# Performance work log

Measured on AMD Instinct MI355X. Metric: run time of the kernel, lower is better.

The kernel has to match this reference:

```python
import jax, jax.numpy as jnp
import numpy as np

EDGE_WIDTH = 128
NUM_HEADS = 8
LN_EPS = 1e-5


def setup_inputs() -> dict:
    key = jax.random.key(0)
    ks = jax.random.split(key, 8)
    B, N, C, H = 2, 512, EDGE_WIDTH, NUM_HEADS
    e = jax.random.normal(ks[0], (B, N, N, C), dtype=jnp.float32)
    mask = jnp.zeros((B, N, N, 1), dtype=jnp.float32)
    s = 0.05
    return {
        "e": e,
        "mask": mask,
        "ln_w": jnp.ones((C,), dtype=jnp.float32),
        "ln_b": jnp.zeros((C,), dtype=jnp.float32),
        "Wv": jax.random.normal(ks[1], (C, 4 * H), dtype=jnp.float32) * s,
        "bv": jnp.zeros((4 * H,), dtype=jnp.float32),
        "We": jax.random.normal(ks[2], (C, 4 * H), dtype=jnp.float32) * s,
        "be": jnp.zeros((4 * H,), dtype=jnp.float32),
        "Wo": jax.random.normal(ks[3], (2 * H, 2 * C), dtype=jnp.float32) * s,
        "bo": jnp.zeros((2 * C,), dtype=jnp.float32),
    }


def siglin(g, l):
    return jax.nn.sigmoid(g) * l


def reference(e, mask, ln_w, ln_b, Wv, bv, We, be, Wo, bo):
    H = NUM_HEADS
    # LayerNorm over edge_width
    mu = jnp.mean(e, axis=-1, keepdims=True)
    var = jnp.var(e, axis=-1, keepdims=True)
    e_ln = (e - mu) * jax.lax.rsqrt(var + LN_EPS) * ln_w + ln_b
    V = e_ln @ Wv + bv
    E = e_ln @ We + be
    V_in_g, V_in_l, V_out_g, V_out_l = jnp.split(V, 4, axis=-1)
    E_in_g, E_in_l, E_out_g, E_out_l = jnp.split(E, 4, axis=-1)
    V_in = siglin(V_in_g + mask, V_in_l)
    V_out = siglin(V_out_g + mask, V_out_l)
    E_in = siglin(E_in_g + mask, E_in_l)
    E_out = siglin(E_out_g + mask, E_out_l)
    # triangular updates: contract over k per head
    Va_in = jnp.einsum('bikh,bjkh->bijh', E_in, V_in)
    Va_out = jnp.einsum('bkih,bkjh->bijh', E_out, V_out)
    Va = jnp.concatenate([Va_in, Va_out], axis=-1)  # [B,N,N,2H]
    O = Va @ Wo + bo  # [B,N,N,2C]
    e_g, e_l = jnp.split(O, 2, axis=-1)
    return siglin(e_g, e_l)
```

## Files before the change

kernel.cpp:

```cpp
#include <hip/hip_runtime.h>
#include <stdint.h>

#define N_    512
#define C_    128
#define NN_   (N_ * N_)
#define ROWS_ (2 * NN_)
#define GATE_ ((long)2 * 8 * NN_)

typedef __attribute__((ext_vector_type(8))) short short8;
typedef __attribute__((ext_vector_type(4))) float f32x4;
typedef __attribute__((ext_vector_type(4))) unsigned uint4_t;
typedef __attribute__((ext_vector_type(2))) unsigned uint2_t;
typedef unsigned short u16;

static __device__ __forceinline__ u16 f2bf(float f) {
    union { float f; unsigned u; } v; v.f = f;
    unsigned r = v.u + 0x7fffu + ((v.u >> 16) & 1u);
    return (u16)(r >> 16);
}
static __device__ __forceinline__ float bf2f(u16 h) {
    union { unsigned u; float f; } v; v.u = ((unsigned)h) << 16;
    return v.f;
}
static __device__ __forceinline__ float sigmoidf_(float x) {
    return __builtin_amdgcn_rcpf(1.0f + __expf(-x));
}

__global__ __launch_bounds__(256) void k_prep(
    const float* __restrict__ Wv, const float* __restrict__ We,
    const float* __restrict__ Wo, u16* __restrict__ WB, u16* __restrict__ WoB)
{
    int gid = blockIdx.x * 256 + threadIdx.x;
    if (gid < 1024) {
        int chunk = gid >> 6, li = gid & 63;
        int kc = chunk >> 2, ct = chunk & 3;
        int qq = li >> 4, nn = li & 15, c = ct * 16 + nn;
        short8 v;
#pragma unroll
        for (int j = 0; j < 8; ++j) {
            int k = kc * 32 + qq * 8 + j;
            float w = (c < 32) ? Wv[k * 32 + c] : We[k * 32 + (c - 32)];
            v[j] = (short)f2bf(w);
        }
        *(short8*)(&WB[gid * 8]) = v;
    } else if (gid < 3072) {
        int g = gid - 1024;
        int ctp = g >> 6, li = g & 63;
        int ct = ctp & 15, part = ctp >> 4;
        int qq = li >> 4, nn = li & 15, col = ct * 16 + nn;
        short8 v;
#pragma unroll
        for (int j = 0; j < 8; ++j) {
            int k = qq * 8 + j;
            if (k < 16) {
                float w = Wo[k * 256 + col];
                u16 hi = f2bf(w);
                v[j] = part ? (short)f2bf(w - bf2f(hi)) : (short)hi;
            } else v[j] = 0;
        }
        *(short8*)(&WoB[g * 8]) = v;
    }
}

__global__ __launch_bounds__(256) void k_lnproj(
    const float* __restrict__ e, const float* __restrict__ mask,
    const float* __restrict__ lnw, const float* __restrict__ lnb,
    const float* __restrict__ bv, const float* __restrict__ be,
    const u16* __restrict__ WB,
    u16* __restrict__ Vin, u16* __restrict__ Vout,
    u16* __restrict__ Ein, u16* __restrict__ Eout)
{
    const int t = threadIdx.x;
    const int w = t >> 6, l = t & 63;
    const int l15 = l & 15, q = l >> 4;
    const long R0 = (long)blockIdx.x * 64;

    const long Rg = R0 + w * 16 + l15;
    const float* erow = e + Rg * C_ + q * 8;
    float x[32];
#pragma unroll
    for (int kc = 0; kc < 4; ++kc) {
        float4 a = *(const float4*)(erow + kc * 32);
        float4 b = *(const float4*)(erow + kc * 32 + 4);
        x[kc*8+0] = a.x; x[kc*8+1] = a.y; x[kc*8+2] = a.z; x[kc*8+3] = a.w;
        x[kc*8+4] = b.x; x[kc*8+5] = b.y; x[kc*8+6] = b.z; x[kc*8+7] = b.w;
    }
    float s = 0.f, s2 = 0.f;
#pragma unroll
    for (int i = 0; i < 32; ++i) { s += x[i]; s2 += x[i] * x[i]; }
    s  += __shfl_xor(s, 16);  s2 += __shfl_xor(s2, 16);
    s  += __shfl_xor(s, 32);  s2 += __shfl_xor(s2, 32);
    float mu   = s * (1.f / 128.f);
    float var  = s2 * (1.f / 128.f) - mu * mu;
    float rstd = rsqrtf(var + 1e-5f);

    short8 af[4];
#pragma unroll
    for (int kc = 0; kc < 4; ++kc) {
        const float* lwp = lnw + kc * 32 + q * 8;
        const float* lbp = lnb + kc * 32 + q * 8;
        float4 w0 = *(const float4*)lwp, w1 = *(const float4*)(lwp + 4);
        float4 b0 = *(const float4*)lbp, b1 = *(const float4*)(lbp + 4);
        float ww[8] = {w0.x,w0.y,w0.z,w0.w,w1.x,w1.y,w1.z,w1.w};
        float bb[8] = {b0.x,b0.y,b0.z,b0.w,b1.x,b1.y,b1.z,b1.w};
#pragma unroll
        for (int j = 0; j < 8; ++j)
            af[kc][j] = (short)f2bf((x[kc*8+j] - mu) * rstd * ww[j] + bb[j]);
    }

    f32x4 acc[4];
#pragma unroll
    for (int ct = 0; ct < 4; ++ct) acc[ct] = (f32x4){0.f, 0.f, 0.f, 0.f};
#pragma unroll
    for (int kc = 0; kc < 4; ++kc) {
#pragma unroll
        for (int ct = 0; ct < 4; ++ct) {
            short8 bf = *(const short8*)(WB + ((kc * 4 + ct) * 64 + l) * 8);
            acc[ct] = __builtin_amdgcn_mfma_f32_16x16x32_bf16(af[kc], bf, acc[ct], 0, 0, 0);
        }
    }

    float mrow[4];
#pragma unroll
    for (int r = 0; r < 4; ++r) mrow[r] = mask[R0 + w * 16 + q * 4 + r];
    const bool is_gate = (l15 & 8) == 0;
    const int h = l15 & 7;
    const long bb_ = R0 >> 18;
    const long rem0 = (R0 & (NN_ - 1)) + w * 16 + q * 4;
    u16* bufs[4] = { Vin, Vout, Ein, Eout };
#pragma unroll
    for (int ct = 0; ct < 4; ++ct) {
        int cc = (ct * 16 + l15) & 31;
        float bias = (ct < 2) ? bv[cc] : be[cc];
        float vals[4];
#pragma unroll
        for (int r = 0; r < 4; ++r) {
            float val = acc[ct][r] + bias;
            float partner = __shfl_xor(val, 8);
            vals[r] = partner * sigmoidf_(val + mrow[r]);
        }
        if (is_gate) {
            uint2_t p;
            p[0] = (unsigned)f2bf(vals[0]) | ((unsigned)f2bf(vals[1]) << 16);
            p[1] = (unsigned)f2bf(vals[2]) | ((unsigned)f2bf(vals[3]) << 16);
            *(uint2_t*)(bufs[ct] + (bb_ * 8 + h) * (long)NN_ + rem0) = p;
        }
    }
}

__global__ __launch_bounds__(256) void k_tri(
    const u16* __restrict__ Vin, const u16* __restrict__ Vout,
    const u16* __restrict__ Ein, const u16* __restrict__ Eout,
    u16* __restrict__ Va)
{
    __shared__ __align__(16) u16 lA[128 * 72];
    __shared__ __align__(16) u16 lB[128 * 72];
    const int bid = blockIdx.x;
    const int tj = bid & 3, ti = (bid >> 2) & 3, fl = (bid >> 4) & 1;
    const int h = (bid >> 5) & 7, b = (bid >> 8) & 1;
    const u16* Ap = (fl ? Eout : Ein) + (long)(b * 8 + h) * NN_;
    const u16* Bp = (fl ? Vout : Vin) + (long)(b * 8 + h) * NN_;
    u16* Cp = Va + (long)(b * 16 + fl * 8 + h) * NN_;

    const int t = threadIdx.x;
    const int w = t >> 6, l = t & 63, l15 = l & 15, q = l >> 4;
    const int rt = (w >> 1) * 64, ctl = (w & 1) * 64;

    f32x4 acc[4][4];
#pragma unroll
    for (int rr = 0; rr < 4; ++rr)
#pragma unroll
        for (int cc = 0; cc < 4; ++cc) acc[rr][cc] = (f32x4){0.f, 0.f, 0.f, 0.f};

    for (int ks = 0; ks < 512; ks += 64) {
        if (fl == 0) {
#pragma unroll
            for (int p = 0; p < 4; ++p) {
                int cid = t + p * 256;
                int r = cid >> 3, seg = cid & 7;
                *(uint4_t*)(&lA[r * 72 + seg * 8]) =
                    *(const uint4_t*)(Ap + (long)(ti * 128 + r) * 512 + ks + seg * 8);
                *(uint4_t*)(&lB[r * 72 + seg * 8]) =
                    *(const uint4_t*)(Bp + (long)(tj * 128 + r) * 512 + ks + seg * 8);
            }
        } else {
            const u16* P = (t < 128) ? Ap : Bp;
            u16* L = (t < 128) ? lA : lB;
            const int tt = t & 127, ib = tt & 15, kb = tt >> 4;
            const int io = ((t < 128) ? ti : tj) * 128 + ib * 8;
            uint4_t o[8];
#pragma unroll
            for (int p2 = 0; p2 < 4; ++p2) {
                uint4_t ra = *(const uint4_t*)(P + (long)(ks + kb * 8 + 2 * p2    ) * 512 + io);
                uint4_t rb = *(const uint4_t*)(P + (long)(ks + kb * 8 + 2 * p2 + 1) * 512 + io);
#pragma unroll
                for (int d = 0; d < 4; ++d) {
                    o[2*d  ][p2] = __builtin_amdgcn_perm(rb[d], ra[d], 0x05040100u);
                    o[2*d+1][p2] = __builtin_amdgcn_perm(rb[d], ra[d], 0x07060302u);
                }
            }
#pragma unroll
            for (int j = 0; j < 8; ++j)
                *(uint4_t*)(&L[(ib * 8 + j) * 72 + kb * 8]) = o[j];
        }
        __syncthreads();
#pragma unroll
        for (int kf = 0; kf < 2; ++kf) {
            short8 a[4], bf[4];
#pragma unroll
            for (int rr = 0; rr < 4; ++rr)
                a[rr] = *(const short8*)(&lA[(rt + rr * 16 + l15) * 72 + kf * 32 + q * 8]);
#pragma unroll
            for (int cc = 0; cc < 4; ++cc)
                bf[cc] = *(const short8*)(&lB[(ctl + cc * 16 + l15) * 72 + kf * 32 + q * 8]);
#pragma unroll
            for (int rr = 0; rr < 4; ++rr)
#pragma unroll
                for (int cc = 0; cc < 4; ++cc)
                    acc[rr][cc] = __builtin_amdgcn_mfma_f32_16x16x32_bf16(a[rr], bf[cc], acc[rr][cc], 0, 0, 0);
        }
        __syncthreads();
    }
#pragma unroll
    for (int rr = 0; rr < 4; ++rr)
#pragma unroll
        for (int cc = 0; cc < 4; ++cc)
#pragma unroll
            for (int r = 0; r < 4; ++r) {
                int row = ti * 128 + rt + rr * 16 + q * 4 + r;
                int col = tj * 128 + ctl + cc * 16 + l15;
                Cp[(long)row * 512 + col] = f2bf(acc[rr][cc][r]);
            }
}

__global__ __launch_bounds__(256) void k_out(
    const u16* __restrict__ Va, const u16* __restrict__ WoB,
    const float* __restrict__ bo, float* __restrict__ out)
{
    __shared__ __align__(16) u16 lWoB[2048 * 8];
    __shared__ __align__(16) u16 lVa[64 * 32];
    const int t = threadIdx.x;
    const int w = t >> 6, l = t & 63, l15 = l & 15, q = l >> 4;
    const long R0 = (long)blockIdx.x * 64;
    const long bb = R0 >> 18;
    const long rem0 = R0 & (NN_ - 1);

#pragma unroll
    for (int i2 = 0; i2 < 8; ++i2)
        ((uint4_t*)lWoB)[i2 * 256 + t] = ((const uint4_t*)WoB)[i2 * 256 + t];
    {
        int p = t >> 2, j4 = (t & 3) * 4;
        uint2_t z; z[0] = 0; z[1] = 0;
        *(uint2_t*)(&lVa[p * 32 + 16 + j4]) = z;
    }
    {
        int ch = t >> 4, p0 = (t & 15) * 4;
        uint2_t v = *(const uint2_t*)(Va + (bb * 16 + ch) * (long)NN_ + rem0 + p0);
        u16* pv = (u16*)&v;
#pragma unroll
        for (int i = 0; i < 4; ++i) lVa[(p0 + i) * 32 + ch] = pv[i];
    }
    __syncthreads();

    short8 af = *(const short8*)(&lVa[(w * 16 + l15) * 32 + q * 8]);
    f32x4 acc[16];
#pragma unroll
    for (int ct = 0; ct < 16; ++ct) acc[ct] = (f32x4){0.f, 0.f, 0.f, 0.f};
#pragma unroll
    for (int ct = 0; ct < 16; ++ct) {
        short8 bh = *(const short8*)(&lWoB[(ct * 64 + l) * 8]);
        short8 blo = *(const short8*)(&lWoB[((16 + ct) * 64 + l) * 8]);
        acc[ct] = __builtin_amdgcn_mfma_f32_16x16x32_bf16(af, bh, acc[ct], 0, 0, 0);
        acc[ct] = __builtin_amdgcn_mfma_f32_16x16x32_bf16(af, blo, acc[ct], 0, 0, 0);
    }

#pragma unroll
    for (int ct = 0; ct < 8; ++ct) {
        int cg = ct * 16 + l15;
        float bg = bo[cg], bl = bo[128 + cg];
#pragma unroll
        for (int r = 0; r < 4; ++r) {
            int row = w * 16 + q * 4 + r;
            float g  = acc[ct][r] + bg;
            float lv = acc[ct + 8][r] + bl;
            out[(R0 + row) * 128 + cg] = lv * sigmoidf_(g);
        }
    }
}

extern "C" void kernel_launch(void* const* d_in, const int* in_sizes, int n_in,
                              void* d_out, int out_size, void* d_ws, size_t ws_size,
                              hipStream_t stream)
{
    const float* e    = (const float*)d_in[0];
    const float* mask = (const float*)d_in[1];
    const float* lnw  = (const float*)d_in[2];
    const float* lnb  = (const float*)d_in[3];
    const float* Wv   = (const float*)d_in[4];
    const float* bv   = (const float*)d_in[5];
    const float* We   = (const float*)d_in[6];
    const float* be   = (const float*)d_in[7];
    const float* Wo   = (const float*)d_in[8];
    const float* bo   = (const float*)d_in[9];
    float* out = (float*)d_out;

    u16* ws   = (u16*)d_ws;
    u16* Ein  = ws;
    u16* Vin  = ws + 1L * GATE_;
    u16* Eout = ws + 2L * GATE_;
    u16* Vout = ws + 3L * GATE_;
    u16* Va   = ws + 4L * GATE_;
    u16* WB   = ws + 6L * GATE_;
    u16* WoB  = WB + 8192;

    hipLaunchKernelGGL(k_prep, dim3(12), dim3(256), 0, stream, Wv, We, Wo, WB, WoB);
    hipLaunchKernelGGL(k_lnproj, dim3(ROWS_ / 64), dim3(256), 0, stream,
                       e, mask, lnw, lnb, bv, be, WB, Vin, Vout, Ein, Eout);
    hipLaunchKernelGGL(k_tri, dim3(512), dim3(256), 0, stream,
                       Vin, Vout, Ein, Eout, Va);
    hipLaunchKernelGGL(k_out, dim3(ROWS_ / 64), dim3(256), 0, stream,
                       Va, WoB, bo, out);
}
```

Measured before the change: 510.5 us.

## Use direct global-to-LDS loads with XOR swizzle in tri kernel; 32x32 MFMA output kernel

In the triangular kernel, the fl==0 tile load now uses global_load_lds to write straight into LDS, skipping the register round-trip. Padded LDS rows are replaced by an XOR swizzle so reads stay free of bank conflicts. The output kernel drops LDS staging, reads Va straight into MFMA operands and uses 32x32x16 MFMAs over 128 rows per block, which halves the wasted zero-padded K. Risks are strided per-element global reads of Va in k_out and correctness of the swizzle mapping with global_load_lds lane addressing.

```diff
diff --git a/kernel.cpp b/kernel.cpp
--- a/kernel.cpp
+++ b/kernel.cpp
@@ -9,6 +9,7 @@
 
 typedef __attribute__((ext_vector_type(8))) short short8;
 typedef __attribute__((ext_vector_type(4))) float f32x4;
+typedef __attribute__((ext_vector_type(16))) float f32x16;
 typedef __attribute__((ext_vector_type(4))) unsigned uint4_t;
 typedef __attribute__((ext_vector_type(2))) unsigned uint2_t;
 typedef unsigned short u16;
@@ -24,6 +25,11 @@
 }
 static __device__ __forceinline__ float sigmoidf_(float x) {
     return __builtin_amdgcn_rcpf(1.0f + __expf(-x));
+}
+static __device__ __forceinline__ void gl_lds16(const u16* g, u16* l) {
+    __builtin_amdgcn_global_load_lds(
+        (const __attribute__((address_space(1))) unsigned int*)g,
+        (__attribute__((address_space(3))) unsigned int*)l, 16, 0, 0);
 }
 
 __global__ __launch_bounds__(256) void k_prep(
@@ -43,20 +49,18 @@
             v[j] = (short)f2bf(w);
         }
         *(short8*)(&WB[gid * 8]) = v;
-    } else if (gid < 3072) {
+    } else if (gid < 2048) {
         int g = gid - 1024;
-        int ctp = g >> 6, li = g & 63;
-        int ct = ctp & 15, part = ctp >> 4;
-        int qq = li >> 4, nn = li & 15, col = ct * 16 + nn;
+        int grp = g >> 6, li = g & 63;
+        int ct = grp & 7, part = grp >> 3;
+        int col = ct * 32 + (li & 31);
+        int kh = (li >> 5) * 8;
         short8 v;
 #pragma unroll
         for (int j = 0; j < 8; ++j) {
-            int k = qq * 8 + j;
-            if (k < 16) {
-                float w = Wo[k * 256 + col];
-                u16 hi = f2bf(w);
-                v[j] = part ? (short)f2bf(w - bf2f(hi)) : (short)hi;
-            } else v[j] = 0;
+            float w = Wo[(kh + j) * 256 + col];
+            u16 hi = f2bf(w);
+            v[j] = part ? (short)f2bf(w - bf2f(hi)) : (short)hi;
         }
         *(short8*)(&WoB[g * 8]) = v;
     }
@@ -153,8 +157,8 @@
     const u16* __restrict__ Ein, const u16* __restrict__ Eout,
     u16* __restrict__ Va)
 {
-    __shared__ __align__(16) u16 lA[128 * 72];
-    __shared__ __align__(16) u16 lB[128 * 72];
+    __shared__ __align__(16) u16 lA[128 * 64];
+    __shared__ __align__(16) u16 lB[128 * 64];
     const int bid = blockIdx.x;
     const int tj = bid & 3, ti = (bid >> 2) & 3, fl = (bid >> 4) & 1;
     const int h = (bid >> 5) & 7, b = (bid >> 8) & 1;
@@ -176,12 +180,12 @@
         if (fl == 0) {
 #pragma unroll
             for (int p = 0; p < 4; ++p) {
-                int cid = t + p * 256;
-                int r = cid >> 3, seg = cid & 7;
-                *(uint4_t*)(&lA[r * 72 + seg * 8]) =
-                    *(const uint4_t*)(Ap + (long)(ti * 128 + r) * 512 + ks + seg * 8);
-                *(uint4_t*)(&lB[r * 72 + seg * 8]) =
-                    *(const uint4_t*)(Bp + (long)(tj * 128 + r) * 512 + ks + seg * 8);
+                const int cid = p * 256 + t;
+                const int r = cid >> 3, sct = cid & 7;
+                const int sk = ((sct ^ ((r ^ (r >> 3)) & 7)) << 3);
+                const int lbase = (p * 256 + (t & 192)) << 3;
+                gl_lds16(Ap + (long)(ti * 128 + r) * 512 + ks + sk, &lA[lbase]);
+                gl_lds16(Bp + (long)(tj * 128 + r) * 512 + ks + sk, &lB[lbase]);
             }
         } else {
             const u16* P = (t < 128) ? Ap : Bp;
@@ -200,19 +204,27 @@
                 }
             }
 #pragma unroll
-            for (int j = 0; j < 8; ++j)
-                *(uint4_t*)(&L[(ib * 8 + j) * 72 + kb * 8]) = o[j];
+            for (int j = 0; j < 8; ++j) {
+                const int R = ib * 8 + j;
+                const int sl = kb ^ ((R ^ (R >> 3)) & 7);
+                *(uint4_t*)(&L[(R << 6) + (sl << 3)]) = o[j];
+            }
         }
         __syncthreads();
 #pragma unroll
         for (int kf = 0; kf < 2; ++kf) {
+            const int S = kf * 4 + q;
             short8 a[4], bf[4];
 #pragma unroll
-            for (int rr = 0; rr < 4; ++rr)
-                a[rr] = *(const short8*)(&lA[(rt + rr * 16 + l15) * 72 + kf * 32 + q * 8]);
-#pragma unroll
-            for (int cc = 0; cc < 4; ++cc)
-                bf[cc] = *(const short8*)(&lB[(ctl + cc * 16 + l15) * 72 + kf * 32 + q * 8]);
+            for (int rr = 0; rr < 4; ++rr) {
+                const int R = rt + rr * 16 + l15;
+                a[rr] = *(const short8*)(&lA[(R << 6) + ((S ^ ((R ^ (R >> 3)) & 7)) << 3)]);
+            }
+#pragma unroll
+            for (int cc = 0; cc < 4; ++cc) {
+                const int R = ctl + cc * 16 + l15;
+                bf[cc] = *(const short8*)(&lB[(R << 6) + ((S ^ ((R ^ (R >> 3)) & 7)) << 3)]);
+            }
 #pragma unroll
             for (int rr = 0; rr < 4; ++rr)
 #pragma unroll
@@ -237,53 +249,42 @@
     const u16* __restrict__ Va, const u16* __restrict__ WoB,
     const float* __restrict__ bo, float* __restrict__ out)
 {
-    __shared__ __align__(16) u16 lWoB[2048 * 8];
-    __shared__ __align__(16) u16 lVa[64 * 32];
     const int t = threadIdx.x;
-    const int w = t >> 6, l = t & 63, l15 = l & 15, q = l >> 4;
-    const long R0 = (long)blockIdx.x * 64;
+    const int w = t >> 6, l = t & 63;
+    const int l31 = l & 31, hl = l >> 5;
+    const long R0 = (long)blockIdx.x * 128;
     const long bb = R0 >> 18;
-    const long rem0 = R0 & (NN_ - 1);
-
-#pragma unroll
-    for (int i2 = 0; i2 < 8; ++i2)
-        ((uint4_t*)lWoB)[i2 * 256 + t] = ((const uint4_t*)WoB)[i2 * 256 + t];
-    {
-        int p = t >> 2, j4 = (t & 3) * 4;
-        uint2_t z; z[0] = 0; z[1] = 0;
-        *(uint2_t*)(&lVa[p * 32 + 16 + j4]) = z;
-    }
-    {
-        int ch = t >> 4, p0 = (t & 15) * 4;
-        uint2_t v = *(const uint2_t*)(Va + (bb * 16 + ch) * (long)NN_ + rem0 + p0);
-        u16* pv = (u16*)&v;
-#pragma unroll
-        for (int i = 0; i < 4; ++i) lVa[(p0 + i) * 32 + ch] = pv[i];
-    }
-    __syncthreads();
-
-    short8 af = *(const short8*)(&lVa[(w * 16 + l15) * 32 + q * 8]);
-    f32x4 acc[16];
-#pragma unroll
-    for (int ct = 0; ct < 16; ++ct) acc[ct] = (f32x4){0.f, 0.f, 0.f, 0.f};
-#pragma unroll
-    for (int ct = 0; ct < 16; ++ct) {
-        short8 bh = *(const short8*)(&lWoB[(ct * 64 + l) * 8]);
-        short8 blo = *(const short8*)(&lWoB[((16 + ct) * 64 + l) * 8]);
-        acc[ct] = __builtin_amdgcn_mfma_f32_16x16x32_bf16(af, bh, acc[ct], 0, 0, 0);
-        acc[ct] = __builtin_amdgcn_mfma_f32_16x16x32_bf16(af, blo, acc[ct], 0, 0, 0);
-    }
+    const long rem = (R0 & (NN_ - 1)) + w * 32 + l31;
+
+    const u16* vp = Va + (bb * 16 + hl * 8) * (long)NN_ + rem;
+    short8 af;
+#pragma unroll
+    for (int j = 0; j < 8; ++j) af[j] = (short)vp[(long)j * NN_];
+
+    f32x16 acc[8];
+#pragma unroll
+    for (int ct = 0; ct < 8; ++ct)
+#pragma unroll
+        for (int i = 0; i < 16; ++i) acc[ct][i] = 0.f;
 
 #pragma unroll
     for (int ct = 0; ct < 8; ++ct) {
-        int cg = ct * 16 + l15;
-        float bg = bo[cg], bl = bo[128 + cg];
-#pragma unroll
-        for (int r = 0; r < 4; ++r) {
-            int row = w * 16 + q * 4 + r;
-            float g  = acc[ct][r] + bg;
-            float lv = acc[ct + 8][r] + bl;
-            out[(R0 + row) * 128 + cg] = lv * sigmoidf_(g);
+        short8 bh = *(const short8*)(WoB + ((ct    ) * 64 + l) * 8);
+        short8 bl = *(const short8*)(WoB + ((8 + ct) * 64 + l) * 8);
+        acc[ct] = __builtin_amdgcn_mfma_f32_32x32x16_bf16(af, bh, acc[ct], 0, 0, 0);
+        acc[ct] = __builtin_amdgcn_mfma_f32_32x32x16_bf16(af, bl, acc[ct], 0, 0, 0);
+    }
+
+#pragma unroll
+    for (int ct = 0; ct < 4; ++ct) {
+        const int cg = ct * 32 + l31;
+        const float bg = bo[cg], bln = bo[128 + cg];
+#pragma unroll
+        for (int r = 0; r < 16; ++r) {
+            const int rowc = (r & 3) + 8 * (r >> 2) + 4 * hl;
+            const float g  = acc[ct][r] + bg;
+            const float lv = acc[ct + 4][r] + bln;
+            out[(R0 + w * 32 + rowc) * 128 + cg] = lv * sigmoidf_(g);
         }
     }
 }
@@ -313,11 +314,11 @@
     u16* WB   = ws + 6L * GATE_;
     u16* WoB  = WB + 8192;
 
-    hipLaunchKernelGGL(k_prep, dim3(12), dim3(256), 0, stream, Wv, We, Wo, WB, WoB);
+    hipLaunchKernelGGL(k_prep, dim3(8), dim3(256), 0, stream, Wv, We, Wo, WB, WoB);
     hipLaunchKernelGGL(k_lnproj, dim3(ROWS_ / 64), dim3(256), 0, stream,
                        e, mask, lnw, lnb, bv, be, WB, Vin, Vout, Ein, Eout);
     hipLaunchKernelGGL(k_tri, dim3(512), dim3(256), 0, stream,
                        Vin, Vout, Ein, Eout, Va);
-    hipLaunchKernelGGL(k_out, dim3(ROWS_ / 64), dim3(256), 0, stream,
+    hipLaunchKernelGGL(k_out, dim3(ROWS_ / 128), dim3(256), 0, stream,
                        Va, WoB, bo, out);
 }
```

New measurement: 513.9 us. No clear change (+0.7%).
